# Performance work log

Hardware: AMD Instinct MI355X
Metric: run time of the kernel (lower is better)

## Reference

```python
import jax, jax.numpy as jnp
import numpy as np
import math

N_NODES = 50000
N_FEAT = 512
HIDDEN = 512
N_CLUSTERS = 16
N_EDGES = 1600000
CLUSTER_REG = 1.0


def setup_inputs() -> dict:
    key = jax.random.key(0)
    ks = jax.random.split(key, 8)
    src = jax.random.randint(ks[0], (N_EDGES,), 0, N_NODES, dtype=jnp.int32)
    dst = jax.random.randint(ks[1], (N_EDGES,), 0, N_NODES, dtype=jnp.int32)
    graph_vals = jnp.ones((N_EDGES,), dtype=jnp.float32)
    gnorm_vals = jax.random.uniform(ks[2], (N_EDGES,), dtype=jnp.float32)
    features = jax.random.normal(ks[3], (N_NODES, N_FEAT), dtype=jnp.float32)
    # GCN params (DGI-style GCN: Linear(in,out,bias=False) + bias param)
    W = jax.random.normal(ks[4], (N_FEAT, HIDDEN), dtype=jnp.float32) * (1.0 / math.sqrt(N_FEAT))
    b = jnp.zeros((HIDDEN,), dtype=jnp.float32)
    # transform: Linear(architecture, n_clusters), orthogonal-init approximated by scaled normal
    Wt = jax.random.normal(ks[5], (HIDDEN, N_CLUSTERS), dtype=jnp.float32) * (math.sqrt(2.0) / math.sqrt(HIDDEN))
    bt = jnp.zeros((N_CLUSTERS,), dtype=jnp.float32)
    return {"src": src, "dst": dst, "graph_vals": graph_vals, "gnorm_vals": gnorm_vals,
            "features": features, "W": W, "b": b, "Wt": Wt, "bt": bt}


def reference(src, dst, graph_vals, gnorm_vals, features, W, b, Wt, bt):
    N = features.shape[0]
    E = src.shape[0]  # static nnz
    K = Wt.shape[1]
    # GCN: selu(spmm(graph_normalised, X @ W) + b)   (dropout inactive in eval)
    xw = features @ W                                   # [N, H]
    prop = jax.ops.segment_sum(gnorm_vals[:, None] * xw[dst], src, num_segments=N)  # [N, H]
    gcn_out = jax.nn.selu(prop + b)
    # cluster assignments
    assignments = jax.nn.softmax(gcn_out @ Wt + bt, axis=1)  # [N, K]
    # degrees = column sums of sparse graph (torch.sparse.sum dim=0)
    degrees = jax.ops.segment_sum(graph_vals, dst, num_segments=N)[:, None]  # [N, 1]
    # graph_pooled = (A @ S).T @ S
    As = jax.ops.segment_sum(graph_vals[:, None] * assignments[dst], src, num_segments=N)  # [N, K]
    graph_pooled = As.T @ assignments  # [K, K]
    normalizer_left = assignments.T @ degrees          # [K, 1]
    normalizer = (normalizer_left @ normalizer_left.T) / 2.0 / E
    spectral_loss = -jnp.trace(graph_pooled - normalizer) / 2.0 / E
    cluster_sizes = jnp.sum(assignments, axis=0)       # [K]
    cluster_loss = (jnp.linalg.norm(cluster_sizes) / N * math.sqrt(float(K)) - 1.0) * CLUSTER_REG
    return spectral_loss + cluster_loss
```

## Files before the change

### kernel.cpp

```cpp
#include <hip/hip_runtime.h>
#include <math.h>

#define NN 50000
#define NF 512
#define NH 512
#define NK 16

typedef __attribute__((ext_vector_type(8))) short bf16x8;
typedef __attribute__((ext_vector_type(4))) float f32x4;
typedef __attribute__((ext_vector_type(2))) float f32x2;

#define RPART 128
#define TPART 2048

__device__ __forceinline__ unsigned short f2bf(float f) {
  unsigned u = __float_as_uint(f);
  unsigned r = (u + 0x7fffu + ((u >> 16) & 1u)) >> 16;
  return (unsigned short)r;
}

__global__ __launch_bounds__(256) void conv_feat(const float* __restrict__ X,
                                                 unsigned short* __restrict__ Xb, int n4) {
  for (int i = blockIdx.x * blockDim.x + threadIdx.x; i < n4; i += gridDim.x * blockDim.x) {
    float4 v = *(const float4*)(X + (size_t)i * 4);
    ushort4 o;
    o.x = f2bf(v.x); o.y = f2bf(v.y); o.z = f2bf(v.z); o.w = f2bf(v.w);
    *(ushort4*)(Xb + (size_t)i * 4) = o;
  }
}

__global__ __launch_bounds__(256) void conv_w(const float* __restrict__ W,
                                              unsigned short* __restrict__ Bp) {
  int idx = blockIdx.x * blockDim.x + threadIdx.x;
  int k = idx >> 9, col = idx & 511;
  Bp[((size_t)(k >> 3) * 512 + col) * 8 + (k & 7)] = f2bf(W[idx]);
}

#define GBM 128
#define GBN 128
#define GBK 32

__global__ __launch_bounds__(256) void gemm_bf16(const unsigned short* __restrict__ A,
                                                 const unsigned short* __restrict__ Bp,
                                                 unsigned char* __restrict__ C8, int M) {
  __shared__ bf16x8 Abuf[512];
  __shared__ bf16x8 Bbuf[512];
  const int tid = threadIdx.x;
  const int lane = tid & 63;
  const int w = tid >> 6;
  const int wr = w >> 1, wc = w & 1;
  const int bm0 = blockIdx.y * GBM;
  const int bn0 = blockIdx.x * GBN;

  f32x4 acc[4][4];
#pragma unroll
  for (int m = 0; m < 4; ++m)
#pragma unroll
    for (int n = 0; n < 4; ++n)
      acc[m][n] = (f32x4){0.f, 0.f, 0.f, 0.f};

  for (int k0 = 0; k0 < NF; k0 += GBK) {
#pragma unroll
    for (int c = 0; c < 2; ++c) {
      int slot = c * 256 + tid;
      int kc = slot >> 7;
      int rc = slot & 127;
      int gr = bm0 + rc; if (gr > M - 1) gr = M - 1;
      Abuf[slot] = *(const bf16x8*)(A + (size_t)gr * NF + k0 + kc * 8);
      int kcg = (k0 >> 3) + kc;
      Bbuf[slot] = *(const bf16x8*)(Bp + ((size_t)kcg * NH + bn0 + rc) * 8);
    }
    __syncthreads();
    bf16x8 af[4], bfr[4];
#pragma unroll
    for (int m = 0; m < 4; ++m)
      af[m] = Abuf[(lane >> 4) * 128 + wr * 64 + m * 16 + (lane & 15)];
#pragma unroll
    for (int n = 0; n < 4; ++n)
      bfr[n] = Bbuf[(lane >> 4) * 128 + wc * 64 + n * 16 + (lane & 15)];
#pragma unroll
    for (int m = 0; m < 4; ++m)
#pragma unroll
      for (int n = 0; n < 4; ++n)
        acc[m][n] = __builtin_amdgcn_mfma_f32_16x16x32_bf16(af[m], bfr[n], acc[m][n], 0, 0, 0);
    __syncthreads();
  }
#pragma unroll
  for (int m = 0; m < 4; ++m) {
    int grow_base = bm0 + wr * 64 + m * 16 + (lane >> 4) * 4;
#pragma unroll
    for (int r = 0; r < 4; ++r) {
      int grow = grow_base + r;
#pragma unroll
      for (int n = 0; n < 4; ++n) {
        int gcol = bn0 + wc * 64 + n * 16 + (lane & 15);
        int pk = __builtin_amdgcn_cvt_pk_fp8_f32(acc[m][n][r], 0.f, 0, false);
        C8[(size_t)grow * NH + gcol] = (unsigned char)(pk & 0xFF);
      }
    }
  }
}

__global__ void hist_kernel(const int* __restrict__ src, const int* __restrict__ dst,
                            const float* __restrict__ gv, int* __restrict__ counts,
                            float* __restrict__ deg, int E) {
  int e = blockIdx.x * blockDim.x + threadIdx.x;
  if (e < E) {
    atomicAdd(&counts[src[e]], 1);
    atomicAdd(&deg[dst[e]], gv[e]);
  }
}

__global__ __launch_bounds__(1024) void scan_kernel(const int* __restrict__ counts,
                                                    int* __restrict__ offs,
                                                    int* __restrict__ cursor, int n) {
  __shared__ int wsum[16];
  __shared__ int carry_sh;
  const int lane = threadIdx.x & 63;
  const int wave = threadIdx.x >> 6;
  if (threadIdx.x == 0) carry_sh = 0;
  __syncthreads();
  for (int base = 0; base < n; base += 4096) {
    int i0 = base + threadIdx.x * 4;
    int c0 = 0, c1 = 0, c2 = 0, c3 = 0;
    if (i0 + 3 < n) {
      int4 v = *(const int4*)(counts + i0);
      c0 = v.x; c1 = v.y; c2 = v.z; c3 = v.w;
    } else {
      if (i0 < n)     c0 = counts[i0];
      if (i0 + 1 < n) c1 = counts[i0 + 1];
      if (i0 + 2 < n) c2 = counts[i0 + 2];
      if (i0 + 3 < n) c3 = counts[i0 + 3];
    }
    int s = c0 + c1 + c2 + c3;
    int x = s;
#pragma unroll
    for (int d = 1; d < 64; d <<= 1) {
      int y = __shfl_up(x, d, 64);
      if (lane >= d) x += y;
    }
    if (lane == 63) wsum[wave] = x;
    __syncthreads();
    if (wave == 0 && lane < 16) {
      int w = wsum[lane];
      int xx = w;
#pragma unroll
      for (int d = 1; d < 16; d <<= 1) {
        int y = __shfl_up(xx, d, 16);
        if (lane >= d) xx += y;
      }
      wsum[lane] = xx - w;
    }
    __syncthreads();
    int exc = carry_sh + wsum[wave] + x - s;
    if (i0 < n)     { offs[i0]     = exc;                cursor[i0]     = exc; }
    if (i0 + 1 < n) { offs[i0 + 1] = exc + c0;           cursor[i0 + 1] = exc + c0; }
    if (i0 + 2 < n) { offs[i0 + 2] = exc + c0 + c1;      cursor[i0 + 2] = exc + c0 + c1; }
    if (i0 + 3 < n) { offs[i0 + 3] = exc + c0 + c1 + c2; cursor[i0 + 3] = exc + c0 + c1 + c2; }
    __syncthreads();
    if (threadIdx.x == 1023) carry_sh = carry_sh + wsum[15] + x;
    __syncthreads();
  }
  if (threadIdx.x == 0) offs[n] = carry_sh;
}

__global__ void scatter_kernel(const int* __restrict__ src, const int* __restrict__ dst,
                               const float* __restrict__ gn, int* __restrict__ cursor,
                               int2* __restrict__ epair, int E) {
  int e = blockIdx.x * blockDim.x + threadIdx.x;
  if (e < E) {
    int pos = atomicAdd(&cursor[src[e]], 1);
    int2 v; v.x = dst[e]; v.y = __float_as_int(gn[e]);
    epair[pos] = v;
  }
}

__global__ __launch_bounds__(256) void node_kernel(const unsigned* __restrict__ xw8,
                                                   const int* __restrict__ offs,
                                                   const int2* __restrict__ epair,
                                                   const float* __restrict__ bias,
                                                   const float* __restrict__ Wt,
                                                   const float* __restrict__ bt,
                                                   float* __restrict__ assign, int n) {
  __shared__ int sk[256];
  __shared__ float sv[256];
  __shared__ int ok[256];
  __shared__ float ov[256];
  __shared__ float cmb[128][4];
  __shared__ float red[2][NK];
  int node = blockIdx.x;
  if (node >= n) return;
  const int t = threadIdx.x;
  const int hl = t & 127;
  const int q = t >> 7;
  const int beg = offs[node], end = offs[node + 1];

  float a0 = 0.f, a1 = 0.f, a2 = 0.f, a3 = 0.f;

  for (int cbeg = beg; cbeg < end; cbeg += 256) {
    int d = end - cbeg; if (d > 256) d = 256;
    if (t < d) { int2 p = epair[cbeg + t]; sk[t] = p.x; sv[t] = __int_as_float(p.y); }
    __syncthreads();
    if (t < d) {
      int k = sk[t];
      int rank = 0;
      for (int j = 0; j < d; ++j) {
        int kj = sk[j];
        rank += (kj < k) || (kj == k && j < t);
      }
      ok[rank] = k; ov[rank] = sv[t];
    }
    __syncthreads();
#define ACC(V, G)                                                     \
    { f32x2 lo = __builtin_amdgcn_cvt_pk_f32_fp8(V, false);           \
      f32x2 hi = __builtin_amdgcn_cvt_pk_f32_fp8(V, true);            \
      a0 = fmaf(G, lo[0], a0); a1 = fmaf(G, lo[1], a1);               \
      a2 = fmaf(G, hi[0], a2); a3 = fmaf(G, hi[1], a3); }
    int nf = d & ~7;
    for (int b = 0; b < nf; b += 8) {
      int e0 = b + q, e1 = b + 2 + q, e2 = b + 4 + q, e3 = b + 6 + q;
      int i0 = ok[e0], i1 = ok[e1], i2 = ok[e2], i3 = ok[e3];
      unsigned v0 = xw8[(size_t)i0 * 128 + hl];
      unsigned v1 = xw8[(size_t)i1 * 128 + hl];
      unsigned v2 = xw8[(size_t)i2 * 128 + hl];
      unsigned v3 = xw8[(size_t)i3 * 128 + hl];
      float g0 = ov[e0], g1 = ov[e1], g2 = ov[e2], g3 = ov[e3];
      ACC(v0, g0) ACC(v1, g1) ACC(v2, g2) ACC(v3, g3)
    }
    for (int e = nf + q; e < d; e += 2) {
      unsigned v = xw8[(size_t)ok[e] * 128 + hl];
      float g = ov[e];
      ACC(v, g)
    }
#undef ACC
    __syncthreads();
  }

  if (q == 1) { cmb[hl][0] = a0; cmb[hl][1] = a1; cmb[hl][2] = a2; cmb[hl][3] = a3; }
  __syncthreads();
  if (q == 0) {
    a0 += cmb[hl][0]; a1 += cmb[hl][1]; a2 += cmb[hl][2]; a3 += cmb[hl][3];
    float a[4] = {a0, a1, a2, a3};
    const float SC = 1.0507009873554805f, AL = 1.6732632423543772f;
    float p[NK];
#pragma unroll
    for (int k = 0; k < NK; ++k) p[k] = 0.f;
#pragma unroll
    for (int j = 0; j < 4; ++j) {
      int dim = hl * 4 + j;
      float v = a[j] + bias[dim];
      v = (v > 0.f) ? SC * v : SC * AL * (expf(v) - 1.f);
      const float* wrow = Wt + (size_t)dim * NK;
#pragma unroll
      for (int k = 0; k < NK; ++k) p[k] = fmaf(v, wrow[k], p[k]);
    }
#pragma unroll
    for (int off = 32; off >= 1; off >>= 1)
#pragma unroll
      for (int k = 0; k < NK; ++k) p[k] += __shfl_down(p[k], off, 64);
    int wave = t >> 6, lane = t & 63;
    if (lane == 0) {
#pragma unroll
      for (int k = 0; k < NK; ++k) red[wave][k] = p[k];
    }
  }
  __syncthreads();
  if (t < NK) {
    float l = red[0][t] + red[1][t] + bt[t];
    float m = l;
#pragma unroll
    for (int off = 8; off >= 1; off >>= 1) m = fmaxf(m, __shfl_xor(m, off, 16));
    float ex = expf(l - m);
    float s = ex;
#pragma unroll
    for (int off = 8; off >= 1; off >>= 1) s += __shfl_xor(s, off, 16);
    assign[(size_t)node * NK + t] = ex / s;
  }
}

__global__ __launch_bounds__(256) void reduce_cs_nl(const float* __restrict__ assign,
                                                    const float* __restrict__ deg,
                                                    float* __restrict__ P1, int n) {
  __shared__ float lds[4][32];
  float cs[NK] = {}, nl[NK] = {};
  for (int i = blockIdx.x * blockDim.x + threadIdx.x; i < n; i += gridDim.x * blockDim.x) {
    float d = deg[i];
    const float4* ap = (const float4*)(assign + (size_t)i * NK);
#pragma unroll
    for (int q = 0; q < 4; ++q) {
      float4 a = ap[q];
      cs[q * 4 + 0] += a.x; cs[q * 4 + 1] += a.y;
      cs[q * 4 + 2] += a.z; cs[q * 4 + 3] += a.w;
      nl[q * 4 + 0] = fmaf(a.x, d, nl[q * 4 + 0]);
      nl[q * 4 + 1] = fmaf(a.y, d, nl[q * 4 + 1]);
      nl[q * 4 + 2] = fmaf(a.z, d, nl[q * 4 + 2]);
      nl[q * 4 + 3] = fmaf(a.w, d, nl[q * 4 + 3]);
    }
  }
#pragma unroll
  for (int off = 32; off >= 1; off >>= 1) {
#pragma unroll
    for (int k = 0; k < NK; ++k) {
      cs[k] += __shfl_down(cs[k], off, 64);
      nl[k] += __shfl_down(nl[k], off, 64);
    }
  }
  int wave = threadIdx.x >> 6, lane = threadIdx.x & 63;
  if (lane == 0) {
#pragma unroll
    for (int k = 0; k < NK; ++k) { lds[wave][k] = cs[k]; lds[wave][NK + k] = nl[k]; }
  }
  __syncthreads();
  if (threadIdx.x < 32)
    P1[(size_t)blockIdx.x * 32 + threadIdx.x] =
        lds[0][threadIdx.x] + lds[1][threadIdx.x] + lds[2][threadIdx.x] + lds[3][threadIdx.x];
}

__global__ __launch_bounds__(256) void trace_kernel(const int* __restrict__ src,
                                                    const int* __restrict__ dst,
                                                    const float* __restrict__ gv,
                                                    const float* __restrict__ assign,
                                                    float* __restrict__ T2, int E) {
  __shared__ float lds[4];
  float t = 0.f;
  for (int e = blockIdx.x * blockDim.x + threadIdx.x; e < E; e += gridDim.x * blockDim.x) {
    int s = src[e], d = dst[e];
    const float4* as = (const float4*)(assign + (size_t)s * NK);
    const float4* ad = (const float4*)(assign + (size_t)d * NK);
    float dot = 0.f;
#pragma unroll
    for (int q = 0; q < 4; ++q) {
      float4 x = as[q], y = ad[q];
      dot += x.x * y.x + x.y * y.y + x.z * y.z + x.w * y.w;
    }
    t = fmaf(gv[e], dot, t);
  }
#pragma unroll
  for (int off = 32; off >= 1; off >>= 1) t += __shfl_down(t, off, 64);
  int wave = threadIdx.x >> 6, lane = threadIdx.x & 63;
  if (lane == 0) lds[wave] = t;
  __syncthreads();
  if (threadIdx.x == 0) T2[blockIdx.x] = lds[0] + lds[1] + lds[2] + lds[3];
}

__global__ __launch_bounds__(256) void final_kernel(const float* __restrict__ P1,
                                                    const float* __restrict__ T2,
                                                    float* __restrict__ out,
                                                    int np1, int np2, int E, int n) {
  __shared__ float arr[256];
  __shared__ float csnl[32];
  const int t = threadIdx.x;
  float s = 0.f;
  for (int p = (t >> 5); p < np1; p += 8) s += P1[(size_t)p * 32 + (t & 31)];
  arr[t] = s;
  __syncthreads();
  if (t < 32) {
    float v = 0.f;
#pragma unroll
    for (int j = 0; j < 8; ++j) v += arr[t + j * 32];
    csnl[t] = v;
  }
  __syncthreads();
  float tv = 0.f;
  for (int p = t; p < np2; p += 256) tv += T2[p];
  arr[t] = tv;
  __syncthreads();
  if (t == 0) {
    float tp = 0.f;
    for (int j = 0; j < 256; ++j) tp += arr[j];
    float sc = 0.f, sn = 0.f;
#pragma unroll
    for (int k = 0; k < NK; ++k) {
      sc += csnl[k] * csnl[k];
      sn += csnl[NK + k] * csnl[NK + k];
    }
    float twoE = 2.0f * (float)E;
    float spectral = -(tp - sn / twoE) / twoE;
    float closs = (sqrtf(sc) / (float)n) * 4.0f - 1.0f;
    out[0] = spectral + closs;
  }
}

extern "C" void kernel_launch(void* const* d_in, const int* in_sizes, int n_in,
                              void* d_out, int out_size, void* d_ws, size_t ws_size,
                              hipStream_t stream) {
  const int*   src  = (const int*)d_in[0];
  const int*   dst  = (const int*)d_in[1];
  const float* gv   = (const float*)d_in[2];
  const float* gn   = (const float*)d_in[3];
  const float* feat = (const float*)d_in[4];
  const float* W    = (const float*)d_in[5];
  const float* b    = (const float*)d_in[6];
  const float* Wt   = (const float*)d_in[7];
  const float* bt   = (const float*)d_in[8];
  const int E = in_sizes[0];
  const int N = in_sizes[4] / NF;
  const int Mblocks = (N + GBM - 1) / GBM;
  const int Mpad = Mblocks * GBM;

  char* ws = (char*)d_ws;
  size_t off = 0;
  auto alloc = [&](size_t bytes) {
    void* p = ws + off;
    off += (bytes + 255) & ~(size_t)255;
    return p;
  };
  unsigned short* feat_bf = (unsigned short*)alloc((size_t)N * NF * sizeof(unsigned short));
  unsigned short* Wp      = (unsigned short*)alloc((size_t)NF * NH * sizeof(unsigned short));
  unsigned char*  xw8     = (unsigned char*)alloc((size_t)Mpad * NH);
  int*   counts = (int*)alloc((size_t)N * sizeof(int));
  int*   offs   = (int*)alloc((size_t)(N + 1) * sizeof(int));
  int*   cursor = (int*)alloc((size_t)N * sizeof(int));
  float* deg    = (float*)alloc((size_t)N * sizeof(float));
  int2*  epair  = (int2*)alloc((size_t)E * sizeof(int2));
  float* assign = (float*)alloc((size_t)N * NK * sizeof(float));
  float* P1     = (float*)alloc((size_t)RPART * 32 * sizeof(float));
  float* T2     = (float*)alloc((size_t)TPART * sizeof(float));
  (void)ws_size; (void)n_in; (void)out_size;

  hipMemsetAsync(counts, 0, (size_t)N * sizeof(int), stream);
  hipMemsetAsync(deg, 0, (size_t)N * sizeof(float), stream);

  conv_feat<<<2048, 256, 0, stream>>>(feat, feat_bf, N * NF / 4);
  conv_w<<<(NF * NH) / 256, 256, 0, stream>>>(W, Wp);

  dim3 ggrid(NH / GBN, Mblocks);
  gemm_bf16<<<ggrid, 256, 0, stream>>>(feat_bf, Wp, xw8, N);

  int eblocks = (E + 255) / 256;
  hist_kernel<<<eblocks, 256, 0, stream>>>(src, dst, gv, counts, deg, E);
  scan_kernel<<<1, 1024, 0, stream>>>(counts, offs, cursor, N);
  scatter_kernel<<<eblocks, 256, 0, stream>>>(src, dst, gn, cursor, epair, E);

  node_kernel<<<N, 256, 0, stream>>>((const unsigned*)xw8, offs, epair, b, Wt, bt, assign, N);

  reduce_cs_nl<<<RPART, 256, 0, stream>>>(assign, deg, P1, N);
  trace_kernel<<<TPART, 256, 0, stream>>>(src, dst, gv, assign, T2, E);
  final_kernel<<<1, 256, 0, stream>>>(P1, T2, (float*)d_out, RPART, TPART, E, N);
}
```

Measured before the change: 710.5 us.

## Split SpMM node aggregation into feature slices across blocks, separate softmax kernel

The per-node aggregation now launches a grid of one block per node per 64-wide feature slice, 8 slices in all, and each block writes partial cluster logits. A new kernel sums the partial logits and applies the softmax. The in-block O(d^2) rank sort of neighbour indices is removed. Each block gathers only 64 bytes per neighbour row, and 16 edge groups work in parallel to expose more memory-level parallelism. The cost is 8x more blocks, each re-reading the edge list, plus an extra intermediate buffer and kernel launch.

New measurement: 961.4 us. +35.3%, slower.

```diff
diff --git a/kernel.cpp b/kernel.cpp
--- a/kernel.cpp
+++ b/kernel.cpp
@@ -5,6 +5,7 @@
 #define NF 512
 #define NH 512
 #define NK 16
+#define NSLICE 8
 
 typedef __attribute__((ext_vector_type(8))) short bf16x8;
 typedef __attribute__((ext_vector_type(4))) float f32x4;
@@ -175,25 +176,22 @@
   }
 }
 
-__global__ __launch_bounds__(256) void node_kernel(const unsigned* __restrict__ xw8,
-                                                   const int* __restrict__ offs,
-                                                   const int2* __restrict__ epair,
-                                                   const float* __restrict__ bias,
-                                                   const float* __restrict__ Wt,
-                                                   const float* __restrict__ bt,
-                                                   float* __restrict__ assign, int n) {
+__global__ __launch_bounds__(256) void slice_kernel(const unsigned* __restrict__ xw8,
+                                                    const int* __restrict__ offs,
+                                                    const int2* __restrict__ epair,
+                                                    const float* __restrict__ bias,
+                                                    const float* __restrict__ Wt,
+                                                    float* __restrict__ plg, int n) {
   __shared__ int sk[256];
   __shared__ float sv[256];
-  __shared__ int ok[256];
-  __shared__ float ov[256];
-  __shared__ float cmb[128][4];
-  __shared__ float red[2][NK];
-  int node = blockIdx.x;
-  if (node >= n) return;
+  __shared__ float cmb[16][17][4];
+  const int node = blockIdx.x;
+  const int slice = blockIdx.y;
   const int t = threadIdx.x;
-  const int hl = t & 127;
-  const int q = t >> 7;
+  const int eg = t >> 4;
+  const int dw = t & 15;
   const int beg = offs[node], end = offs[node + 1];
+  const unsigned* base = xw8 + slice * 16 + dw;
 
   float a0 = 0.f, a1 = 0.f, a2 = 0.f, a3 = 0.f;
 
@@ -201,81 +199,64 @@
     int d = end - cbeg; if (d > 256) d = 256;
     if (t < d) { int2 p = epair[cbeg + t]; sk[t] = p.x; sv[t] = __int_as_float(p.y); }
     __syncthreads();
-    if (t < d) {
-      int k = sk[t];
-      int rank = 0;
-      for (int j = 0; j < d; ++j) {
-        int kj = sk[j];
-        rank += (kj < k) || (kj == k && j < t);
-      }
-      ok[rank] = k; ov[rank] = sv[t];
-    }
-    __syncthreads();
-#define ACC(V, G)                                                     \
-    { f32x2 lo = __builtin_amdgcn_cvt_pk_f32_fp8(V, false);           \
-      f32x2 hi = __builtin_amdgcn_cvt_pk_f32_fp8(V, true);            \
-      a0 = fmaf(G, lo[0], a0); a1 = fmaf(G, lo[1], a1);               \
-      a2 = fmaf(G, hi[0], a2); a3 = fmaf(G, hi[1], a3); }
-    int nf = d & ~7;
-    for (int b = 0; b < nf; b += 8) {
-      int e0 = b + q, e1 = b + 2 + q, e2 = b + 4 + q, e3 = b + 6 + q;
-      int i0 = ok[e0], i1 = ok[e1], i2 = ok[e2], i3 = ok[e3];
-      unsigned v0 = xw8[(size_t)i0 * 128 + hl];
-      unsigned v1 = xw8[(size_t)i1 * 128 + hl];
-      unsigned v2 = xw8[(size_t)i2 * 128 + hl];
-      unsigned v3 = xw8[(size_t)i3 * 128 + hl];
-      float g0 = ov[e0], g1 = ov[e1], g2 = ov[e2], g3 = ov[e3];
-      ACC(v0, g0) ACC(v1, g1) ACC(v2, g2) ACC(v3, g3)
-    }
-    for (int e = nf + q; e < d; e += 2) {
-      unsigned v = xw8[(size_t)ok[e] * 128 + hl];
-      float g = ov[e];
-      ACC(v, g)
-    }
-#undef ACC
-    __syncthreads();
-  }
-
-  if (q == 1) { cmb[hl][0] = a0; cmb[hl][1] = a1; cmb[hl][2] = a2; cmb[hl][3] = a3; }
-  __syncthreads();
-  if (q == 0) {
-    a0 += cmb[hl][0]; a1 += cmb[hl][1]; a2 += cmb[hl][2]; a3 += cmb[hl][3];
-    float a[4] = {a0, a1, a2, a3};
+    for (int e = eg; e < d; e += 16) {
+      int dn = sk[e];
+      float g = sv[e];
+      unsigned v = base[(size_t)dn * 128];
+      f32x2 lo = __builtin_amdgcn_cvt_pk_f32_fp8(v, false);
+      f32x2 hi = __builtin_amdgcn_cvt_pk_f32_fp8(v, true);
+      a0 = fmaf(g, lo[0], a0); a1 = fmaf(g, lo[1], a1);
+      a2 = fmaf(g, hi[0], a2); a3 = fmaf(g, hi[1], a3);
+    }
+    __syncthreads();
+  }
+
+  cmb[eg][dw][0] = a0; cmb[eg][dw][1] = a1;
+  cmb[eg][dw][2] = a2; cmb[eg][dw][3] = a3;
+  __syncthreads();
+
+  if (t < 64) {
+    float s = 0.f;
+#pragma unroll
+    for (int e2 = 0; e2 < 16; ++e2) s += cmb[e2][t >> 2][t & 3];
+    int dim = slice * 64 + t;
+    float v = s + bias[dim];
     const float SC = 1.0507009873554805f, AL = 1.6732632423543772f;
+    v = (v > 0.f) ? SC * v : SC * AL * (expf(v) - 1.f);
     float p[NK];
-#pragma unroll
-    for (int k = 0; k < NK; ++k) p[k] = 0.f;
-#pragma unroll
-    for (int j = 0; j < 4; ++j) {
-      int dim = hl * 4 + j;
-      float v = a[j] + bias[dim];
-      v = (v > 0.f) ? SC * v : SC * AL * (expf(v) - 1.f);
-      const float* wrow = Wt + (size_t)dim * NK;
-#pragma unroll
-      for (int k = 0; k < NK; ++k) p[k] = fmaf(v, wrow[k], p[k]);
-    }
+    const float* wrow = Wt + (size_t)dim * NK;
+#pragma unroll
+    for (int k = 0; k < NK; ++k) p[k] = v * wrow[k];
 #pragma unroll
     for (int off = 32; off >= 1; off >>= 1)
 #pragma unroll
       for (int k = 0; k < NK; ++k) p[k] += __shfl_down(p[k], off, 64);
-    int wave = t >> 6, lane = t & 63;
-    if (lane == 0) {
-#pragma unroll
-      for (int k = 0; k < NK; ++k) red[wave][k] = p[k];
-    }
-  }
-  __syncthreads();
-  if (t < NK) {
-    float l = red[0][t] + red[1][t] + bt[t];
-    float m = l;
-#pragma unroll
-    for (int off = 8; off >= 1; off >>= 1) m = fmaxf(m, __shfl_xor(m, off, 16));
-    float ex = expf(l - m);
-    float s = ex;
-#pragma unroll
-    for (int off = 8; off >= 1; off >>= 1) s += __shfl_xor(s, off, 16);
-    assign[(size_t)node * NK + t] = ex / s;
-  }
+    if (t == 0) {
+      float* o = plg + ((size_t)node * NSLICE + slice) * NK;
+#pragma unroll
+      for (int k = 0; k < NK; ++k) o[k] = p[k];
+    }
+  }
+}
+
+__global__ __launch_bounds__(256) void softmax_kernel(const float* __restrict__ plg,
+                                                      const float* __restrict__ bt,
+                                                      float* __restrict__ assign, int n) {
+  int idx = blockIdx.x * 256 + threadIdx.x;
+  int node = idx >> 4;
+  int k = idx & 15;
+  if (node >= n) return;
+  float l = bt[k];
+#pragma unroll
+  for (int s = 0; s < NSLICE; ++s) l += plg[((size_t)node * NSLICE + s) * NK + k];
+  float m = l;
+#pragma unroll
+  for (int off = 8; off >= 1; off >>= 1) m = fmaxf(m, __shfl_xor(m, off, 16));
+  float ex = expf(l - m);
+  float ssum = ex;
+#pragma unroll
+  for (int off = 8; off >= 1; off >>= 1) ssum += __shfl_xor(ssum, off, 16);
+  assign[idx] = ex / ssum;
 }
 
 __global__ __launch_bounds__(256) void reduce_cs_nl(const float* __restrict__ assign,
@@ -414,6 +395,7 @@
   float* deg    = (float*)alloc((size_t)N * sizeof(float));
   int2*  epair  = (int2*)alloc((size_t)E * sizeof(int2));
   float* assign = (float*)alloc((size_t)N * NK * sizeof(float));
+  float* plg    = (float*)alloc((size_t)N * NSLICE * NK * sizeof(float));
   float* P1     = (float*)alloc((size_t)RPART * 32 * sizeof(float));
   float* T2     = (float*)alloc((size_t)TPART * sizeof(float));
   (void)ws_size; (void)n_in; (void)out_size;
@@ -432,7 +414,9 @@
   scan_kernel<<<1, 1024, 0, stream>>>(counts, offs, cursor, N);
   scatter_kernel<<<eblocks, 256, 0, stream>>>(src, dst, gn, cursor, epair, E);
 
-  node_kernel<<<N, 256, 0, stream>>>((const unsigned*)xw8, offs, epair, b, Wt, bt, assign, N);
+  dim3 sgrid(N, NSLICE);
+  slice_kernel<<<sgrid, 256, 0, stream>>>((const unsigned*)xw8, offs, epair, b, Wt, plg, N);
+  softmax_kernel<<<(N * NK + 255) / 256, 256, 0, stream>>>(plg, bt, assign, N);
 
   reduce_cs_nl<<<RPART, 256, 0, stream>>>(assign, deg, P1, N);
   trace_kernel<<<TPART, 256, 0, stream>>>(src, dst, gv, assign, T2, E);
```

## Parallelize CSR offset scan across blocks and drop per-node neighbor sort

Applied to the files above, without the earlier changes.

Replaces the single-block serial prefix scan over node counts with a three-stage scan: block sums, a one-wave scan of those sums, then a per-block local scan. It also removes the O(d^2) shared-memory rank sort of neighbor indices in the node aggregation kernel and gathers directly in scatter order. This cuts serialized latency and per-node compute, but the floating-point summation order now depends on atomic scatter order, and the scan supports at most 64 blocks.

Measured after the change: 664.5 us. 1.07x faster.

```diff
diff --git a/kernel.cpp b/kernel.cpp
--- a/kernel.cpp
+++ b/kernel.cpp
@@ -111,57 +111,76 @@
   }
 }
 
-__global__ __launch_bounds__(1024) void scan_kernel(const int* __restrict__ counts,
-                                                    int* __restrict__ offs,
-                                                    int* __restrict__ cursor, int n) {
-  __shared__ int wsum[16];
-  __shared__ int carry_sh;
-  const int lane = threadIdx.x & 63;
-  const int wave = threadIdx.x >> 6;
-  if (threadIdx.x == 0) carry_sh = 0;
-  __syncthreads();
-  for (int base = 0; base < n; base += 4096) {
-    int i0 = base + threadIdx.x * 4;
-    int c0 = 0, c1 = 0, c2 = 0, c3 = 0;
-    if (i0 + 3 < n) {
-      int4 v = *(const int4*)(counts + i0);
-      c0 = v.x; c1 = v.y; c2 = v.z; c3 = v.w;
-    } else {
-      if (i0 < n)     c0 = counts[i0];
-      if (i0 + 1 < n) c1 = counts[i0 + 1];
-      if (i0 + 2 < n) c2 = counts[i0 + 2];
-      if (i0 + 3 < n) c3 = counts[i0 + 3];
-    }
-    int s = c0 + c1 + c2 + c3;
-    int x = s;
-#pragma unroll
-    for (int d = 1; d < 64; d <<= 1) {
-      int y = __shfl_up(x, d, 64);
-      if (lane >= d) x += y;
-    }
-    if (lane == 63) wsum[wave] = x;
-    __syncthreads();
-    if (wave == 0 && lane < 16) {
-      int w = wsum[lane];
-      int xx = w;
-#pragma unroll
-      for (int d = 1; d < 16; d <<= 1) {
-        int y = __shfl_up(xx, d, 16);
-        if (lane >= d) xx += y;
-      }
-      wsum[lane] = xx - w;
-    }
-    __syncthreads();
-    int exc = carry_sh + wsum[wave] + x - s;
-    if (i0 < n)     { offs[i0]     = exc;                cursor[i0]     = exc; }
-    if (i0 + 1 < n) { offs[i0 + 1] = exc + c0;           cursor[i0 + 1] = exc + c0; }
-    if (i0 + 2 < n) { offs[i0 + 2] = exc + c0 + c1;      cursor[i0 + 2] = exc + c0 + c1; }
-    if (i0 + 3 < n) { offs[i0 + 3] = exc + c0 + c1 + c2; cursor[i0 + 3] = exc + c0 + c1 + c2; }
-    __syncthreads();
-    if (threadIdx.x == 1023) carry_sh = carry_sh + wsum[15] + x;
-    __syncthreads();
-  }
-  if (threadIdx.x == 0) offs[n] = carry_sh;
+__global__ __launch_bounds__(256) void scanA(const int* __restrict__ counts,
+                                             int* __restrict__ bsum, int n) {
+  __shared__ int ws[4];
+  int i0 = blockIdx.x * 1024 + threadIdx.x * 4;
+  int s = 0;
+  if (i0 + 3 < n) {
+    int4 v = *(const int4*)(counts + i0);
+    s = v.x + v.y + v.z + v.w;
+  } else {
+#pragma unroll
+    for (int j = 0; j < 4; ++j) if (i0 + j < n) s += counts[i0 + j];
+  }
+#pragma unroll
+  for (int off = 32; off >= 1; off >>= 1) s += __shfl_down(s, off, 64);
+  int wv = threadIdx.x >> 6, ln = threadIdx.x & 63;
+  if (ln == 0) ws[wv] = s;
+  __syncthreads();
+  if (threadIdx.x == 0) bsum[blockIdx.x] = ws[0] + ws[1] + ws[2] + ws[3];
+}
+
+__global__ __launch_bounds__(64) void scanB(const int* __restrict__ bsum,
+                                            int* __restrict__ bbase,
+                                            int* __restrict__ offs, int nb, int n) {
+  int ln = threadIdx.x;
+  int v = ln < nb ? bsum[ln] : 0;
+  int x = v;
+#pragma unroll
+  for (int d = 1; d < 64; d <<= 1) {
+    int y = __shfl_up(x, d, 64);
+    if (ln >= d) x += y;
+  }
+  if (ln < nb) bbase[ln] = x - v;
+  if (ln == nb - 1) offs[n] = x;
+}
+
+__global__ __launch_bounds__(256) void scanC(const int* __restrict__ counts,
+                                             const int* __restrict__ bbase,
+                                             int* __restrict__ offs,
+                                             int* __restrict__ cursor, int n) {
+  __shared__ int ws[4];
+  int i0 = blockIdx.x * 1024 + threadIdx.x * 4;
+  int c0 = 0, c1 = 0, c2 = 0, c3 = 0;
+  if (i0 + 3 < n) {
+    int4 v = *(const int4*)(counts + i0);
+    c0 = v.x; c1 = v.y; c2 = v.z; c3 = v.w;
+  } else {
+    if (i0 < n)     c0 = counts[i0];
+    if (i0 + 1 < n) c1 = counts[i0 + 1];
+    if (i0 + 2 < n) c2 = counts[i0 + 2];
+    if (i0 + 3 < n) c3 = counts[i0 + 3];
+  }
+  int s = c0 + c1 + c2 + c3;
+  int x = s;
+  int wv = threadIdx.x >> 6, ln = threadIdx.x & 63;
+#pragma unroll
+  for (int d = 1; d < 64; d <<= 1) {
+    int y = __shfl_up(x, d, 64);
+    if (ln >= d) x += y;
+  }
+  if (ln == 63) ws[wv] = x;
+  __syncthreads();
+  int woff = 0;
+  if (wv > 0) woff += ws[0];
+  if (wv > 1) woff += ws[1];
+  if (wv > 2) woff += ws[2];
+  int exc = bbase[blockIdx.x] + woff + x - s;
+  if (i0 < n)     { offs[i0]     = exc;                cursor[i0]     = exc; }
+  if (i0 + 1 < n) { offs[i0 + 1] = exc + c0;           cursor[i0 + 1] = exc + c0; }
+  if (i0 + 2 < n) { offs[i0 + 2] = exc + c0 + c1;      cursor[i0 + 2] = exc + c0 + c1; }
+  if (i0 + 3 < n) { offs[i0 + 3] = exc + c0 + c1 + c2; cursor[i0 + 3] = exc + c0 + c1 + c2; }
 }
 
 __global__ void scatter_kernel(const int* __restrict__ src, const int* __restrict__ dst,
@@ -184,8 +203,6 @@
                                                    float* __restrict__ assign, int n) {
   __shared__ int sk[256];
   __shared__ float sv[256];
-  __shared__ int ok[256];
-  __shared__ float ov[256];
   __shared__ float cmb[128][4];
   __shared__ float red[2][NK];
   int node = blockIdx.x;
@@ -200,16 +217,6 @@
   for (int cbeg = beg; cbeg < end; cbeg += 256) {
     int d = end - cbeg; if (d > 256) d = 256;
     if (t < d) { int2 p = epair[cbeg + t]; sk[t] = p.x; sv[t] = __int_as_float(p.y); }
-    __syncthreads();
-    if (t < d) {
-      int k = sk[t];
-      int rank = 0;
-      for (int j = 0; j < d; ++j) {
-        int kj = sk[j];
-        rank += (kj < k) || (kj == k && j < t);
-      }
-      ok[rank] = k; ov[rank] = sv[t];
-    }
     __syncthreads();
 #define ACC(V, G)                                                     \
     { f32x2 lo = __builtin_amdgcn_cvt_pk_f32_fp8(V, false);           \
@@ -219,17 +226,17 @@
     int nf = d & ~7;
     for (int b = 0; b < nf; b += 8) {
       int e0 = b + q, e1 = b + 2 + q, e2 = b + 4 + q, e3 = b + 6 + q;
-      int i0 = ok[e0], i1 = ok[e1], i2 = ok[e2], i3 = ok[e3];
+      int i0 = sk[e0], i1 = sk[e1], i2 = sk[e2], i3 = sk[e3];
       unsigned v0 = xw8[(size_t)i0 * 128 + hl];
       unsigned v1 = xw8[(size_t)i1 * 128 + hl];
       unsigned v2 = xw8[(size_t)i2 * 128 + hl];
       unsigned v3 = xw8[(size_t)i3 * 128 + hl];
-      float g0 = ov[e0], g1 = ov[e1], g2 = ov[e2], g3 = ov[e3];
+      float g0 = sv[e0], g1 = sv[e1], g2 = sv[e2], g3 = sv[e3];
       ACC(v0, g0) ACC(v1, g1) ACC(v2, g2) ACC(v3, g3)
     }
     for (int e = nf + q; e < d; e += 2) {
-      unsigned v = xw8[(size_t)ok[e] * 128 + hl];
-      float g = ov[e];
+      unsigned v = xw8[(size_t)sk[e] * 128 + hl];
+      float g = sv[e];
       ACC(v, g)
     }
 #undef ACC
@@ -397,6 +404,7 @@
   const int N = in_sizes[4] / NF;
   const int Mblocks = (N + GBM - 1) / GBM;
   const int Mpad = Mblocks * GBM;
+  const int nsb = (N + 1023) / 1024;
 
   char* ws = (char*)d_ws;
   size_t off = 0;
@@ -416,6 +424,8 @@
   float* assign = (float*)alloc((size_t)N * NK * sizeof(float));
   float* P1     = (float*)alloc((size_t)RPART * 32 * sizeof(float));
   float* T2     = (float*)alloc((size_t)TPART * sizeof(float));
+  int*   bsum   = (int*)alloc(64 * sizeof(int));
+  int*   bbase  = (int*)alloc(64 * sizeof(int));
   (void)ws_size; (void)n_in; (void)out_size;
 
   hipMemsetAsync(counts, 0, (size_t)N * sizeof(int), stream);
@@ -429,7 +439,9 @@
 
   int eblocks = (E + 255) / 256;
   hist_kernel<<<eblocks, 256, 0, stream>>>(src, dst, gv, counts, deg, E);
-  scan_kernel<<<1, 1024, 0, stream>>>(counts, offs, cursor, N);
+  scanA<<<nsb, 256, 0, stream>>>(counts, bsum, N);
+  scanB<<<1, 64, 0, stream>>>(bsum, bbase, offs, nsb, N);
+  scanC<<<nsb, 256, 0, stream>>>(counts, bbase, offs, cursor, N);
   scatter_kernel<<<eblocks, 256, 0, stream>>>(src, dst, gn, cursor, epair, E);
 
   node_kernel<<<N, 256, 0, stream>>>((const unsigned*)xw8, offs, epair, b, Wt, bt, assign, N);
```
